# Optimization experiments

Measured on AMD Instinct MI355X. Metric: run time of the kernel, lower is better.

## Reference

```python
import jax, jax.numpy as jnp
import numpy as np

HEAD_DIM = 64
HIDDEN_SIZE = 3072
NUM_HEADS = 48
B, TXT, VID = 1, 256, 1792
N = TXT + VID


def _layernorm(x, g, b, eps=1e-5):
    mu = jnp.mean(x, axis=-1, keepdims=True)
    xc = x - mu
    var = jnp.mean(xc * xc, axis=-1, keepdims=True)
    return xc * jax.lax.rsqrt(var + eps) * g + b


def _apply_rope1(x, freqs):
    # x: [B, L, H, D]; freqs: [1, 1, Lf, D//2, 2, 2]
    Bx, L, H, D = x.shape
    x_ = x.reshape(Bx, L, H, D // 2, 1, 2)
    # faithful to torch: if dim-2 sizes mismatch (H vs Lf), slice freqs to H
    if x_.shape[2] != 1 and freqs.shape[2] != 1 and x_.shape[2] != freqs.shape[2]:
        freqs = freqs[:, :, : x_.shape[2]]
    out = freqs[..., 0] * x_[..., 0] + freqs[..., 1] * x_[..., 1]
    return out.reshape(Bx, L, H, D).astype(x.dtype)


def setup_inputs() -> dict:
    key = jax.random.key(0)
    ks = jax.random.split(key, 16)
    s = 1.0 / np.sqrt(HIDDEN_SIZE)
    d = dict(
        combined=jax.random.normal(ks[0], (B, N, HIDDEN_SIZE), jnp.float32),
        freqs=jax.random.normal(ks[1], (1, 1, VID, HEAD_DIM // 2, 2, 2), jnp.float32),
        Wq=jax.random.normal(ks[2], (HIDDEN_SIZE, HIDDEN_SIZE), jnp.float32) * s,
        bq=jnp.zeros((HIDDEN_SIZE,), jnp.float32),
        Wk=jax.random.normal(ks[3], (HIDDEN_SIZE, HIDDEN_SIZE), jnp.float32) * s,
        bk=jnp.zeros((HIDDEN_SIZE,), jnp.float32),
        Wv=jax.random.normal(ks[4], (HIDDEN_SIZE, HIDDEN_SIZE), jnp.float32) * s,
        bv=jnp.zeros((HIDDEN_SIZE,), jnp.float32),
        Wo=jax.random.normal(ks[5], (HIDDEN_SIZE, HIDDEN_SIZE), jnp.float32) * s,
        bo=jnp.zeros((HIDDEN_SIZE,), jnp.float32),
        gq=jnp.ones((HEAD_DIM,), jnp.float32),
        bgq=jnp.zeros((HEAD_DIM,), jnp.float32),
        gk=jnp.ones((HEAD_DIM,), jnp.float32),
        bgk=jnp.zeros((HEAD_DIM,), jnp.float32),
        txt_len=TXT,
    )
    return d


def reference(combined, freqs, Wq, bq, Wk, bk, Wv, bv, Wo, bo, gq, bgq, gk, bgk, txt_len):
    Bx, Nx, _ = combined.shape
    Q = (combined @ Wq.T + bq).reshape(Bx, Nx, NUM_HEADS, HEAD_DIM)
    K = (combined @ Wk.T + bk).reshape(Bx, Nx, NUM_HEADS, HEAD_DIM)
    V = (combined @ Wv.T + bv).reshape(Bx, Nx, NUM_HEADS, HEAD_DIM)
    Q = _layernorm(Q, gq, bgq)
    K = _layernorm(K, gk, bgk)
    if freqs is not None and Nx - txt_len > 0:
        Q_vid = _apply_rope1(Q[:, txt_len:], freqs)
        K_vid = _apply_rope1(K[:, txt_len:], freqs)
        Q = jnp.concatenate([Q[:, :txt_len], Q_vid], axis=1)
        K = jnp.concatenate([K[:, :txt_len], K_vid], axis=1)
    # SDPA in fp32: [B, H, N, D]
    q = Q.transpose(0, 2, 1, 3).astype(jnp.float32)
    k = K.transpose(0, 2, 1, 3).astype(jnp.float32)
    v = V.transpose(0, 2, 1, 3).astype(jnp.float32)
    scale = 1.0 / np.sqrt(HEAD_DIM)
    scores = jnp.einsum('bhqd,bhkd->bhqk', q, k) * scale
    probs = jax.nn.softmax(scores, axis=-1)
    attn = jnp.einsum('bhqk,bhkd->bhqd', probs, v).astype(combined.dtype)
    attn = attn.transpose(0, 2, 1, 3).reshape(Bx, Nx, HIDDEN_SIZE)
    out = attn @ Wo.T + bo
    return out[:, txt_len:], out[:, :txt_len]
```

## Files before the change

kernel.cpp:

```cpp
#include <hip/hip_runtime.h>
#include <hip/hip_bf16.h>

typedef __attribute__((ext_vector_type(8))) short bf16x8;
typedef __attribute__((ext_vector_type(4))) float f32x4;
typedef unsigned int __attribute__((address_space(1))) as1_uint;
typedef unsigned int __attribute__((address_space(3))) as3_uint;

#define TXT 256
#define VIDN 1792
#define SEQ 2048
#define HID 3072
#define NH 48
#define HD 64
#define QSCALE 0.18033688011112042f

__device__ __forceinline__ unsigned short f2bf(float f) {
  union { float f; unsigned int u; } x; x.f = f;
  unsigned int r = x.u + 0x7fffu + ((x.u >> 16) & 1u);
  return (unsigned short)(r >> 16);
}

__device__ __forceinline__ void gload16(const void* g, void* l) {
  __builtin_amdgcn_global_load_lds((const as1_uint*)g, (as3_uint*)l, 16, 0, 0);
}

__device__ __forceinline__ void fbar() {
  asm volatile("" ::: "memory");
  __builtin_amdgcn_s_barrier();
  asm volatile("" ::: "memory");
}

__global__ __launch_bounds__(256) void cvt5_kernel(
    const float* __restrict__ comb, const float* __restrict__ wq,
    const float* __restrict__ wk, const float* __restrict__ wv,
    const float* __restrict__ wo,
    unsigned short* __restrict__ abf, unsigned short* __restrict__ wqkv,
    unsigned short* __restrict__ wob) {
  const int CB = (SEQ * HID) / 1024;
  const int WB = (HID * HID) / 1024;
  int bid = blockIdx.x;
  const float* s; unsigned short* d; int r;
  if (bid < CB) { s = comb; d = abf; r = bid; }
  else {
    int q = bid - CB; int m = q / WB; r = q - m * WB;
    if (m < 3) { s = (m == 0) ? wq : (m == 1) ? wk : wv; d = wqkv + (size_t)m * HID * HID; }
    else { s = wo; d = wob; }
  }
  int i = (r * 256 + threadIdx.x) * 4;
  float4 v = *(const float4*)(s + i);
  ushort4 o;
  o.x = f2bf(v.x); o.y = f2bf(v.y); o.z = f2bf(v.z); o.w = f2bf(v.w);
  *(ushort4*)(d + i) = o;
}

template<int MODE>
__global__ __launch_bounds__(512) void gemm8p(
    const unsigned short* __restrict__ A,
    const unsigned short* __restrict__ Bt,
    int K, int ntn,
    float* __restrict__ Cq, unsigned short* __restrict__ Vt, const float* __restrict__ bv,
    float* __restrict__ Cout, const float* __restrict__ bo)
{
  __shared__ unsigned short lds[3 * 24576];
  const int tid = threadIdx.x;
  const int mt = blockIdx.x / ntn, nt = blockIdx.x % ntn;
  const int m0 = mt * 128, n0 = nt * 256;
  const int w = tid >> 6, lane = tid & 63, lr = lane & 15, lg = lane >> 4;
  const int wr = w >> 2, wc = w & 3;
  f32x4 acc[4][4] = {};
  const int NT = K >> 6;

  const unsigned short *As0, *As1, *Bs0, *Bs1, *Bs2, *Bs3;
  int ao0, ao1, bb0, bb1, bb2, bb3;
  {
    int so, ss;
    so = tid * 16;          ss = so ^ (((so >> 7) & 7) << 4);
    ao0 = so; As0 = A + (size_t)(m0 + (ss >> 7)) * K + ((ss & 127) >> 1);
    so = (512 + tid) * 16;  ss = so ^ (((so >> 7) & 7) << 4);
    ao1 = so; As1 = A + (size_t)(m0 + (ss >> 7)) * K + ((ss & 127) >> 1);
    so = tid * 16;          ss = so ^ (((so >> 7) & 7) << 4);
    bb0 = so; Bs0 = Bt + (size_t)(n0 + (ss >> 7)) * K + ((ss & 127) >> 1);
    so = (512 + tid) * 16;  ss = so ^ (((so >> 7) & 7) << 4);
    bb1 = so; Bs1 = Bt + (size_t)(n0 + (ss >> 7)) * K + ((ss & 127) >> 1);
    so = (1024 + tid) * 16; ss = so ^ (((so >> 7) & 7) << 4);
    bb2 = so; Bs2 = Bt + (size_t)(n0 + (ss >> 7)) * K + ((ss & 127) >> 1);
    so = (1536 + tid) * 16; ss = so ^ (((so >> 7) & 7) << 4);
    bb3 = so; Bs3 = Bt + (size_t)(n0 + (ss >> 7)) * K + ((ss & 127) >> 1);
  }

  int ra[2][4], rb[2][4];
#pragma unroll
  for (int h = 0; h < 2; ++h) {
#pragma unroll
    for (int f = 0; f < 4; ++f) {
      int r1 = wr * 64 + f * 16 + lr;
      ra[h][f] = (r1 * 64 + h * 32 + lg * 8) ^ ((r1 & 7) << 3);
      int r2 = wc * 64 + f * 16 + lr;
      rb[h][f] = (r2 * 64 + h * 32 + lg * 8) ^ ((r2 & 7) << 3);
    }
  }

#define STAGE_ALL(t)                                                           \
  {                                                                            \
    char* sb_ = (char*)lds + ((t) % 3) * 49152;                                \
    const int kk_ = (t) << 6;                                                  \
    gload16(As0 + kk_, sb_ + ao0);                                             \
    gload16(As1 + kk_, sb_ + ao1);                                             \
    gload16(Bs0 + kk_, sb_ + 16384 + bb0);                                     \
    gload16(Bs1 + kk_, sb_ + 16384 + bb1);                                     \
    gload16(Bs2 + kk_, sb_ + 16384 + bb2);                                     \
    gload16(Bs3 + kk_, sb_ + 16384 + bb3);                                     \
  }

#define MM8(N0, N1)                                                            \
  __builtin_amdgcn_s_setprio(1);                                               \
  acc[0][N0] = __builtin_amdgcn_mfma_f32_16x16x32_bf16(af0, bq0, acc[0][N0], 0, 0, 0); \
  acc[1][N0] = __builtin_amdgcn_mfma_f32_16x16x32_bf16(af1, bq0, acc[1][N0], 0, 0, 0); \
  acc[2][N0] = __builtin_amdgcn_mfma_f32_16x16x32_bf16(af2, bq0, acc[2][N0], 0, 0, 0); \
  acc[3][N0] = __builtin_amdgcn_mfma_f32_16x16x32_bf16(af3, bq0, acc[3][N0], 0, 0, 0); \
  acc[0][N1] = __builtin_amdgcn_mfma_f32_16x16x32_bf16(af0, bq1, acc[0][N1], 0, 0, 0); \
  acc[1][N1] = __builtin_amdgcn_mfma_f32_16x16x32_bf16(af1, bq1, acc[1][N1], 0, 0, 0); \
  acc[2][N1] = __builtin_amdgcn_mfma_f32_16x16x32_bf16(af2, bq1, acc[2][N1], 0, 0, 0); \
  acc[3][N1] = __builtin_amdgcn_mfma_f32_16x16x32_bf16(af3, bq1, acc[3][N1], 0, 0, 0); \
  __builtin_amdgcn_s_setprio(0);

#define ITER(t, SG, VMC)                                                       \
  {                                                                            \
    const unsigned short* lA = lds + ((t) % 3) * 24576;                        \
    const unsigned short* lB = lA + 8192;                                      \
    char* sb = (char*)lds + (((t) + 2) % 3) * 49152;                           \
    const int kk = ((t) + 2) << 6;                                             \
    bf16x8 af0, af1, af2, af3, bq0, bq1;                                       \
                                                \
    af0 = *(const bf16x8*)&lA[ra[0][0]];                                       \
    af1 = *(const bf16x8*)&lA[ra[0][1]];                                       \
    af2 = *(const bf16x8*)&lA[ra[0][2]];                                       \
    af3 = *(const bf16x8*)&lA[ra[0][3]];                                       \
    bq0 = *(const bf16x8*)&lB[rb[0][0]];                                       \
    bq1 = *(const bf16x8*)&lB[rb[0][1]];                                       \
    if (SG) { gload16(As0 + kk, sb + ao0); gload16(As1 + kk, sb + ao1); }      \
    fbar();                                                                    \
    MM8(0, 1)                                                                  \
    fbar();                                                                    \
                                                \
    bq0 = *(const bf16x8*)&lB[rb[0][2]];                                       \
    bq1 = *(const bf16x8*)&lB[rb[0][3]];                                       \
    if (SG) { gload16(Bs0 + kk, sb + 16384 + bb0);                             \
              gload16(Bs1 + kk, sb + 16384 + bb1); }                           \
    fbar();                                                                    \
    MM8(2, 3)                                                                  \
    fbar();                                                                    \
                                                \
    af0 = *(const bf16x8*)&lA[ra[1][0]];                                       \
    af1 = *(const bf16x8*)&lA[ra[1][1]];                                       \
    af2 = *(const bf16x8*)&lA[ra[1][2]];                                       \
    af3 = *(const bf16x8*)&lA[ra[1][3]];                                       \
    bq0 = *(const bf16x8*)&lB[rb[1][0]];                                       \
    bq1 = *(const bf16x8*)&lB[rb[1][1]];                                       \
    if (SG) { gload16(Bs2 + kk, sb + 16384 + bb2);                             \
              gload16(Bs3 + kk, sb + 16384 + bb3); }                           \
    fbar();                                                                    \
    MM8(0, 1)                                                                  \
    fbar();                                                                    \
                      \
    bq0 = *(const bf16x8*)&lB[rb[1][2]];                                       \
    bq1 = *(const bf16x8*)&lB[rb[1][3]];                                       \
    VMC;                                                                       \
    fbar();                                                                    \
    MM8(2, 3)                                                                  \
    fbar();                                                                    \
  }

  STAGE_ALL(0);
  STAGE_ALL(1);
  asm volatile("s_waitcnt vmcnt(6)" ::: "memory");
  fbar();
  int t = 0;
  for (; t < NT - 2; ++t)
    ITER(t, 1, asm volatile("s_waitcnt vmcnt(6)" ::: "memory"));
  ITER(t, 0, asm volatile("s_waitcnt vmcnt(0)" ::: "memory"));
  ++t;
  ITER(t, 0, ((void)0));
#undef STAGE_ALL
#undef MM8
#undef ITER

  if (MODE == 0) {
    if (n0 < 6144) {
#pragma unroll
      for (int mf = 0; mf < 4; ++mf) {
        int row = m0 + wr * 64 + mf * 16 + lg * 4;
#pragma unroll
        for (int nf = 0; nf < 4; ++nf) {
          int col = n0 + wc * 64 + nf * 16 + lr;
#pragma unroll
          for (int j = 0; j < 4; ++j)
            Cq[(size_t)(row + j) * 6144 + col] = acc[mf][nf][j];
        }
      }
    } else {
#pragma unroll
      for (int mf = 0; mf < 4; ++mf) {
        int srow2 = m0 + wr * 64 + mf * 16 + lg * 4;
#pragma unroll
        for (int nf = 0; nf < 4; ++nf) {
          int n2 = n0 - 6144 + wc * 64 + nf * 16 + lr;
          float b = bv[n2];
          ushort4 pk;
          pk.x = f2bf(acc[mf][nf][0] + b);
          pk.y = f2bf(acc[mf][nf][1] + b);
          pk.z = f2bf(acc[mf][nf][2] + b);
          pk.w = f2bf(acc[mf][nf][3] + b);
          *(ushort4*)(Vt + (size_t)n2 * SEQ + srow2) = pk;
        }
      }
    }
  } else {
#pragma unroll
    for (int mf = 0; mf < 4; ++mf) {
      int row = m0 + wr * 64 + mf * 16 + lg * 4;
#pragma unroll
      for (int nf = 0; nf < 4; ++nf) {
        int col = n0 + wc * 64 + nf * 16 + lr;
        float b = bo[col];
#pragma unroll
        for (int j = 0; j < 4; ++j) {
          int s = row + j;
          int orow = (s >= TXT) ? (s - TXT) : (VIDN + s);
          Cout[(size_t)orow * HID + col] = acc[mf][nf][j] + b;
        }
      }
    }
  }
}

__global__ __launch_bounds__(256) void ln_rope_kernel(
    const float* __restrict__ QK,
    const float* __restrict__ bq, const float* __restrict__ bk,
    const float* __restrict__ gq, const float* __restrict__ bgq,
    const float* __restrict__ gk, const float* __restrict__ bgk,
    const float* __restrict__ freqs,
    unsigned short* __restrict__ Qh, unsigned short* __restrict__ Kh)
{
  int wid = blockIdx.x * 4 + (threadIdx.x >> 6);
  int lane = threadIdx.x & 63;
  int s = wid / 96;
  int rem = wid - s * 96;
  int h = rem >> 1, qk = rem & 1;
  int col = h * 64 + lane;
  float x = QK[(size_t)s * 6144 + qk * 3072 + col] + (qk ? bk[col] : bq[col]);
  float m = x;
#pragma unroll
  for (int msk = 1; msk < 64; msk <<= 1) m += __shfl_xor(m, msk);
  float mu = m * (1.0f / 64.0f);
  float xc = x - mu;
  float v = xc * xc;
#pragma unroll
  for (int msk = 1; msk < 64; msk <<= 1) v += __shfl_xor(v, msk);
  float rstd = rsqrtf(v * (1.0f / 64.0f) + 1e-5f);
  float y = xc * rstd * (qk ? gk[lane] : gq[lane]) + (qk ? bgk[lane] : bgq[lane]);
  if (s >= TXT) {
    float p = __shfl_xor(y, 1);
    float xe = (lane & 1) ? p : y;
    float xo = (lane & 1) ? y : p;
    int base = h * 128 + (lane >> 1) * 4 + (lane & 1) * 2;
    y = freqs[base] * xe + freqs[base + 1] * xo;
  }
  if (!qk) y *= QSCALE;
  (qk ? Kh : Qh)[((size_t)h * SEQ + s) * 64 + lane] = f2bf(y);
}

__global__ __launch_bounds__(512) void fattn_kernel(
    const unsigned short* __restrict__ Qh, const unsigned short* __restrict__ Kh,
    const unsigned short* __restrict__ Vt, unsigned short* __restrict__ ctx)
{
  __shared__ unsigned short kt[2][2][64][32];
  __shared__ unsigned short vt[2][2][64][32];
  __shared__ unsigned short pl[8][16][72];
  const int h = blockIdx.x >> 4;
  const int q0 = (blockIdx.x & 15) * 128;
  const int tid = threadIdx.x, w = tid >> 6, lane = tid & 63, lr = lane & 15, lg = lane >> 4;

  bf16x8 qf0, qf1;
  {
    const unsigned short* qp = Qh + ((size_t)h * SEQ + q0 + w * 16 + lr) * 64 + lg * 8;
    qf0 = *(const bf16x8*)qp;
    qf1 = *(const bf16x8*)(qp + 32);
  }
  f32x4 oacc[4] = {};
  float mrun = -1e30f, lrun = 0.f;

  const int soff = tid * 16;
  const int shalf = soff >> 12;
  const int srem = soff & 4095;
  const int srow = srem >> 6, scb = srem & 63;
  const unsigned short* Ksrc = Kh + ((size_t)h * SEQ + srow) * 64 + shalf * 32 + (scb >> 1);
  const unsigned short* Vsrc = Vt + ((size_t)(h * 64 + srow)) * SEQ + shalf * 32 + (scb >> 1);

#define FSTAGE(t)                                                              \
  {                                                                            \
    const int sl_ = (t) & 1;                                                   \
    const int kv0_ = (t) << 6;                                                 \
    gload16(Ksrc + (size_t)kv0_ * 64, (char*)kt + sl_ * 8192 + soff);          \
    gload16(Vsrc + kv0_, (char*)vt + sl_ * 8192 + soff);                       \
  }

  FSTAGE(0);
  for (int t = 0; t < 32; ++t) {
    const int sl = t & 1;
    if (t < 31) {
      FSTAGE(t + 1);
      asm volatile("s_waitcnt vmcnt(2)" ::: "memory");
    } else {
      asm volatile("s_waitcnt vmcnt(0)" ::: "memory");
    }
    fbar();

    f32x4 sacc[4] = {};
    __builtin_amdgcn_s_setprio(1);
#pragma unroll
    for (int nf = 0; nf < 4; ++nf) {
      bf16x8 a0 = *(const bf16x8*)&kt[sl][0][nf * 16 + lr][lg * 8];
      bf16x8 a1 = *(const bf16x8*)&kt[sl][1][nf * 16 + lr][lg * 8];
      sacc[nf] = __builtin_amdgcn_mfma_f32_16x16x32_bf16(a0, qf0, sacc[nf], 0, 0, 0);
      sacc[nf] = __builtin_amdgcn_mfma_f32_16x16x32_bf16(a1, qf1, sacc[nf], 0, 0, 0);
    }
    __builtin_amdgcn_s_setprio(0);

    float mx;
    {
      float t0 = fmaxf(fmaxf(sacc[0][0], sacc[0][1]), fmaxf(sacc[0][2], sacc[0][3]));
      float t1 = fmaxf(fmaxf(sacc[1][0], sacc[1][1]), fmaxf(sacc[1][2], sacc[1][3]));
      float t2 = fmaxf(fmaxf(sacc[2][0], sacc[2][1]), fmaxf(sacc[2][2], sacc[2][3]));
      float t3 = fmaxf(fmaxf(sacc[3][0], sacc[3][1]), fmaxf(sacc[3][2], sacc[3][3]));
      mx = fmaxf(fmaxf(t0, t1), fmaxf(t2, t3));
    }
    mx = fmaxf(mx, __shfl_xor(mx, 16));
    mx = fmaxf(mx, __shfl_xor(mx, 32));

    if (!__all(mx <= mrun + 8.0f)) {
      float mn = fmaxf(mrun, mx);
      float corr = exp2f(mrun - mn);
      lrun *= corr;
      mrun = mn;
      float c0 = __shfl(corr, lg * 4 + 0);
      float c1 = __shfl(corr, lg * 4 + 1);
      float c2 = __shfl(corr, lg * 4 + 2);
      float c3 = __shfl(corr, lg * 4 + 3);
#pragma unroll
      for (int df = 0; df < 4; ++df) {
        oacc[df][0] *= c0; oacc[df][1] *= c1;
        oacc[df][2] *= c2; oacc[df][3] *= c3;
      }
    }

    float pr[4][4];
#pragma unroll
    for (int nf = 0; nf < 4; ++nf)
#pragma unroll
      for (int r = 0; r < 4; ++r)
        pr[nf][r] = exp2f(sacc[nf][r] - mrun);
    float rs;
    {
      float s0 = (pr[0][0] + pr[0][1]) + (pr[0][2] + pr[0][3]);
      float s1 = (pr[1][0] + pr[1][1]) + (pr[1][2] + pr[1][3]);
      float s2 = (pr[2][0] + pr[2][1]) + (pr[2][2] + pr[2][3]);
      float s3 = (pr[3][0] + pr[3][1]) + (pr[3][2] + pr[3][3]);
      rs = (s0 + s1) + (s2 + s3);
    }
    rs += __shfl_xor(rs, 16);
    rs += __shfl_xor(rs, 32);
    lrun += rs;

#pragma unroll
    for (int nf = 0; nf < 4; ++nf) {
      union { __hip_bfloat162 h; unsigned int u; } c0, c1;
      c0.h = __float22bfloat162_rn(make_float2(pr[nf][0], pr[nf][1]));
      c1.h = __float22bfloat162_rn(make_float2(pr[nf][2], pr[nf][3]));
      uint2 pw; pw.x = c0.u; pw.y = c1.u;
      *(uint2*)&pl[w][lr][nf * 16 + lg * 4] = pw;
    }

    bf16x8 pa0 = *(const bf16x8*)&pl[w][lr][lg * 8];
    bf16x8 pa1 = *(const bf16x8*)&pl[w][lr][32 + lg * 8];
    __builtin_amdgcn_s_setprio(1);
#pragma unroll
    for (int df = 0; df < 4; ++df) {
      bf16x8 v0 = *(const bf16x8*)&vt[sl][0][df * 16 + lr][lg * 8];
      bf16x8 v1 = *(const bf16x8*)&vt[sl][1][df * 16 + lr][lg * 8];
      oacc[df] = __builtin_amdgcn_mfma_f32_16x16x32_bf16(pa0, v0, oacc[df], 0, 0, 0);
      oacc[df] = __builtin_amdgcn_mfma_f32_16x16x32_bf16(pa1, v1, oacc[df], 0, 0, 0);
    }
    __builtin_amdgcn_s_setprio(0);

    fbar();
  }
#undef FSTAGE

  float linv = 1.0f / lrun;
  float i0 = __shfl(linv, lg * 4 + 0);
  float i1 = __shfl(linv, lg * 4 + 1);
  float i2 = __shfl(linv, lg * 4 + 2);
  float i3 = __shfl(linv, lg * 4 + 3);
#pragma unroll
  for (int df = 0; df < 4; ++df) {
    int s = q0 + w * 16 + lg * 4;
    int dcol = h * 64 + df * 16 + lr;
    ctx[(size_t)(s + 0) * HID + dcol] = f2bf(oacc[df][0] * i0);
    ctx[(size_t)(s + 1) * HID + dcol] = f2bf(oacc[df][1] * i1);
    ctx[(size_t)(s + 2) * HID + dcol] = f2bf(oacc[df][2] * i2);
    ctx[(size_t)(s + 3) * HID + dcol] = f2bf(oacc[df][3] * i3);
  }
}

extern "C" void kernel_launch(void* const* d_in, const int* in_sizes, int n_in,
                              void* d_out, int out_size, void* d_ws, size_t ws_size,
                              hipStream_t stream) {
  const float* combined = (const float*)d_in[0];
  const float* freqs    = (const float*)d_in[1];
  const float* Wq  = (const float*)d_in[2];
  const float* bq  = (const float*)d_in[3];
  const float* Wk  = (const float*)d_in[4];
  const float* bk  = (const float*)d_in[5];
  const float* Wv  = (const float*)d_in[6];
  const float* bv  = (const float*)d_in[7];
  const float* Wo  = (const float*)d_in[8];
  const float* bo  = (const float*)d_in[9];
  const float* gq  = (const float*)d_in[10];
  const float* bgq = (const float*)d_in[11];
  const float* gk  = (const float*)d_in[12];
  const float* bgk = (const float*)d_in[13];
  float* out = (float*)d_out;

  char* ws = (char*)d_ws;
  unsigned short* Abf  = (unsigned short*)ws; ws += (size_t)SEQ * HID * 2;
  unsigned short* Wqkv = (unsigned short*)ws; ws += (size_t)3 * HID * HID * 2;
  float*          QK   = (float*)ws;          ws += (size_t)SEQ * 6144 * 4;
  unsigned short* Qh   = (unsigned short*)ws; ws += (size_t)NH * SEQ * HD * 2;
  unsigned short* Kh   = (unsigned short*)ws; ws += (size_t)NH * SEQ * HD * 2;
  unsigned short* Vt   = (unsigned short*)ws; ws += (size_t)NH * HD * SEQ * 2;
  unsigned short* Wob  = (unsigned short*)ws; ws += (size_t)HID * HID * 2;
  unsigned short* ctx  = Abf;

  cvt5_kernel<<<(SEQ * HID) / 1024 + 4 * (HID * HID) / 1024, 256, 0, stream>>>(
      combined, Wq, Wk, Wv, Wo, Abf, Wqkv, Wob);

  gemm8p<0><<<16 * 36, 512, 0, stream>>>(Abf, Wqkv, HID, 36, QK, Vt, bv, nullptr, nullptr);

  ln_rope_kernel<<<(SEQ * NH * 2) / 4, 256, 0, stream>>>(QK, bq, bk, gq, bgq, gk, bgk, freqs, Qh, Kh);

  fattn_kernel<<<NH * 16, 512, 0, stream>>>(Qh, Kh, Vt, ctx);

  gemm8p<1><<<16 * 12, 512, 0, stream>>>(ctx, Wob, HID, 12, nullptr, nullptr, nullptr, out, bo);
}
```

Before: 401.2 us.

## Add dedicated output-projection GEMM with 128x192 tiles to fill all CUs

Replaces the templated reuse of the 128x256 GEMM for the output projection with a new kernel using 128x192 tiles, 256-thread blocks, K-step 32 and a three-stage global-to-LDS pipeline. The grid becomes 256 blocks instead of 192, intended to occupy every compute unit and allow two blocks per CU. The smaller K step adds more barriers per unit of work and uses a new swizzle layout.

```diff
diff --git a/kernel.cpp b/kernel.cpp
--- a/kernel.cpp
+++ b/kernel.cpp
@@ -53,13 +53,11 @@
   *(ushort4*)(d + i) = o;
 }
 
-template<int MODE>
 __global__ __launch_bounds__(512) void gemm8p(
     const unsigned short* __restrict__ A,
     const unsigned short* __restrict__ Bt,
     int K, int ntn,
-    float* __restrict__ Cq, unsigned short* __restrict__ Vt, const float* __restrict__ bv,
-    float* __restrict__ Cout, const float* __restrict__ bo)
+    float* __restrict__ Cq, unsigned short* __restrict__ Vt, const float* __restrict__ bv)
 {
   __shared__ unsigned short lds[3 * 24576];
   const int tid = threadIdx.x;
@@ -131,7 +129,6 @@
     char* sb = (char*)lds + (((t) + 2) % 3) * 49152;                           \
     const int kk = ((t) + 2) << 6;                                             \
     bf16x8 af0, af1, af2, af3, bq0, bq1;                                       \
-                                                \
     af0 = *(const bf16x8*)&lA[ra[0][0]];                                       \
     af1 = *(const bf16x8*)&lA[ra[0][1]];                                       \
     af2 = *(const bf16x8*)&lA[ra[0][2]];                                       \
@@ -142,7 +139,6 @@
     fbar();                                                                    \
     MM8(0, 1)                                                                  \
     fbar();                                                                    \
-                                                \
     bq0 = *(const bf16x8*)&lB[rb[0][2]];                                       \
     bq1 = *(const bf16x8*)&lB[rb[0][3]];                                       \
     if (SG) { gload16(Bs0 + kk, sb + 16384 + bb0);                             \
@@ -150,7 +146,6 @@
     fbar();                                                                    \
     MM8(2, 3)                                                                  \
     fbar();                                                                    \
-                                                \
     af0 = *(const bf16x8*)&lA[ra[1][0]];                                       \
     af1 = *(const bf16x8*)&lA[ra[1][1]];                                       \
     af2 = *(const bf16x8*)&lA[ra[1][2]];                                       \
@@ -162,7 +157,6 @@
     fbar();                                                                    \
     MM8(0, 1)                                                                  \
     fbar();                                                                    \
-                      \
     bq0 = *(const bf16x8*)&lB[rb[1][2]];                                       \
     bq1 = *(const bf16x8*)&lB[rb[1][3]];                                       \
     VMC;                                                                       \
@@ -185,50 +179,143 @@
 #undef MM8
 #undef ITER
 
-  if (MODE == 0) {
-    if (n0 < 6144) {
-#pragma unroll
-      for (int mf = 0; mf < 4; ++mf) {
-        int row = m0 + wr * 64 + mf * 16 + lg * 4;
-#pragma unroll
-        for (int nf = 0; nf < 4; ++nf) {
-          int col = n0 + wc * 64 + nf * 16 + lr;
-#pragma unroll
-          for (int j = 0; j < 4; ++j)
-            Cq[(size_t)(row + j) * 6144 + col] = acc[mf][nf][j];
-        }
-      }
-    } else {
-#pragma unroll
-      for (int mf = 0; mf < 4; ++mf) {
-        int srow2 = m0 + wr * 64 + mf * 16 + lg * 4;
-#pragma unroll
-        for (int nf = 0; nf < 4; ++nf) {
-          int n2 = n0 - 6144 + wc * 64 + nf * 16 + lr;
-          float b = bv[n2];
-          ushort4 pk;
-          pk.x = f2bf(acc[mf][nf][0] + b);
-          pk.y = f2bf(acc[mf][nf][1] + b);
-          pk.z = f2bf(acc[mf][nf][2] + b);
-          pk.w = f2bf(acc[mf][nf][3] + b);
-          *(ushort4*)(Vt + (size_t)n2 * SEQ + srow2) = pk;
-        }
-      }
-    }
-  } else {
+  if (n0 < 6144) {
 #pragma unroll
     for (int mf = 0; mf < 4; ++mf) {
       int row = m0 + wr * 64 + mf * 16 + lg * 4;
 #pragma unroll
       for (int nf = 0; nf < 4; ++nf) {
         int col = n0 + wc * 64 + nf * 16 + lr;
-        float b = bo[col];
-#pragma unroll
-        for (int j = 0; j < 4; ++j) {
-          int s = row + j;
-          int orow = (s >= TXT) ? (s - TXT) : (VIDN + s);
-          Cout[(size_t)orow * HID + col] = acc[mf][nf][j] + b;
-        }
+#pragma unroll
+        for (int j = 0; j < 4; ++j)
+          Cq[(size_t)(row + j) * 6144 + col] = acc[mf][nf][j];
+      }
+    }
+  } else {
+#pragma unroll
+    for (int mf = 0; mf < 4; ++mf) {
+      int srow2 = m0 + wr * 64 + mf * 16 + lg * 4;
+#pragma unroll
+      for (int nf = 0; nf < 4; ++nf) {
+        int n2 = n0 - 6144 + wc * 64 + nf * 16 + lr;
+        float b = bv[n2];
+        ushort4 pk;
+        pk.x = f2bf(acc[mf][nf][0] + b);
+        pk.y = f2bf(acc[mf][nf][1] + b);
+        pk.z = f2bf(acc[mf][nf][2] + b);
+        pk.w = f2bf(acc[mf][nf][3] + b);
+        *(ushort4*)(Vt + (size_t)n2 * SEQ + srow2) = pk;
+      }
+    }
+  }
+}
+
+__global__ __launch_bounds__(256, 2) void gemmF(
+    const unsigned short* __restrict__ A,
+    const unsigned short* __restrict__ Bt,
+    float* __restrict__ Cout, const float* __restrict__ bo)
+{
+  __shared__ unsigned short lds[3 * 10240];
+  const int K = HID;
+  const int tid = threadIdx.x;
+  const int mt = blockIdx.x >> 4, nt = blockIdx.x & 15;
+  const int m0 = mt * 128, n0 = nt * 192;
+  const int w = tid >> 6, lane = tid & 63, lr = lane & 15, lg = lane >> 4;
+  const int wr = w >> 1, wc = w & 1;
+  f32x4 acc[4][6] = {};
+  const int NT = K >> 5;
+
+  const unsigned short* Asrc[2];
+  const unsigned short* Bsrc[3];
+  int aol[2], bol[3];
+#pragma unroll
+  for (int c = 0; c < 2; ++c) {
+    int so = (c * 256 + tid) * 16;
+    aol[c] = so;
+    int ss = so ^ (((so >> 7) & 3) << 4);
+    Asrc[c] = A + (size_t)(m0 + (ss >> 6)) * K + ((ss & 63) >> 1);
+  }
+#pragma unroll
+  for (int c = 0; c < 3; ++c) {
+    int so = (c * 256 + tid) * 16;
+    bol[c] = so;
+    int ss = so ^ (((so >> 7) & 3) << 4);
+    Bsrc[c] = Bt + (size_t)(n0 + (ss >> 6)) * K + ((ss & 63) >> 1);
+  }
+
+  int aoff[4], boff[6];
+#pragma unroll
+  for (int mf = 0; mf < 4; ++mf) {
+    int arow = wr * 64 + mf * 16 + lr;
+    aoff[mf] = arow * 32 + (lg ^ ((arow >> 1) & 3)) * 8;
+  }
+#pragma unroll
+  for (int nf = 0; nf < 6; ++nf) {
+    int brow = wc * 96 + nf * 16 + lr;
+    boff[nf] = brow * 32 + (lg ^ ((brow >> 1) & 3)) * 8;
+  }
+
+#define FSTG(t)                                                                \
+  {                                                                            \
+    char* base_ = (char*)lds + ((t) % 3) * 20480;                              \
+    const int k0_ = (t) << 5;                                                  \
+    gload16(Asrc[0] + k0_, base_ + aol[0]);                                    \
+    gload16(Asrc[1] + k0_, base_ + aol[1]);                                    \
+    gload16(Bsrc[0] + k0_, base_ + 8192 + bol[0]);                             \
+    gload16(Bsrc[1] + k0_, base_ + 8192 + bol[1]);                             \
+    gload16(Bsrc[2] + k0_, base_ + 8192 + bol[2]);                             \
+  }
+
+#define FCMP(t)                                                                \
+  {                                                                            \
+    const unsigned short* lA = lds + ((t) % 3) * 10240;                        \
+    const unsigned short* lB = lA + 4096;                                      \
+    bf16x8 bfr[6];                                                             \
+    _Pragma("unroll")                                                          \
+    for (int nf = 0; nf < 6; ++nf)                                             \
+      bfr[nf] = *(const bf16x8*)&lB[boff[nf]];                                 \
+    __builtin_amdgcn_s_setprio(1);                                             \
+    _Pragma("unroll")                                                          \
+    for (int mf = 0; mf < 4; ++mf) {                                           \
+      bf16x8 af = *(const bf16x8*)&lA[aoff[mf]];                               \
+      _Pragma("unroll")                                                        \
+      for (int nf = 0; nf < 6; ++nf)                                           \
+        acc[mf][nf] = __builtin_amdgcn_mfma_f32_16x16x32_bf16(af, bfr[nf], acc[mf][nf], 0, 0, 0); \
+    }                                                                          \
+    __builtin_amdgcn_s_setprio(0);                                             \
+  }
+
+  FSTG(0); FSTG(1);
+  int t = 0;
+  for (; t < NT - 2; ++t) {
+    FSTG(t + 2);
+    asm volatile("s_waitcnt vmcnt(10)" ::: "memory");
+    fbar();
+    FCMP(t);
+    fbar();
+  }
+  asm volatile("s_waitcnt vmcnt(5)" ::: "memory");
+  fbar();
+  FCMP(t); ++t;
+  fbar();
+  asm volatile("s_waitcnt vmcnt(0)" ::: "memory");
+  fbar();
+  FCMP(t);
+#undef FSTG
+#undef FCMP
+
+#pragma unroll
+  for (int mf = 0; mf < 4; ++mf) {
+    int row = m0 + wr * 64 + mf * 16 + lg * 4;
+#pragma unroll
+    for (int nf = 0; nf < 6; ++nf) {
+      int col = n0 + wc * 96 + nf * 16 + lr;
+      float b = bo[col];
+#pragma unroll
+      for (int j = 0; j < 4; ++j) {
+        int s = row + j;
+        int orow = (s >= TXT) ? (s - TXT) : (VIDN + s);
+        Cout[(size_t)orow * HID + col] = acc[mf][nf][j] + b;
       }
     }
   }
@@ -445,11 +532,11 @@
   cvt5_kernel<<<(SEQ * HID) / 1024 + 4 * (HID * HID) / 1024, 256, 0, stream>>>(
       combined, Wq, Wk, Wv, Wo, Abf, Wqkv, Wob);
 
-  gemm8p<0><<<16 * 36, 512, 0, stream>>>(Abf, Wqkv, HID, 36, QK, Vt, bv, nullptr, nullptr);
+  gemm8p<<<16 * 36, 512, 0, stream>>>(Abf, Wqkv, HID, 36, QK, Vt, bv);
 
   ln_rope_kernel<<<(SEQ * NH * 2) / 4, 256, 0, stream>>>(QK, bq, bk, gq, bgq, gk, bgk, freqs, Qh, Kh);
 
   fattn_kernel<<<NH * 16, 512, 0, stream>>>(Qh, Kh, Vt, ctx);
 
-  gemm8p<1><<<16 * 12, 512, 0, stream>>>(ctx, Wob, HID, 12, nullptr, nullptr, nullptr, out, bo);
-}
+  gemmF<<<16 * 16, 256, 0, stream>>>(ctx, Wob, out, bo);
+}
```

After: 400.9 us. About the same (-0.1%).
